# Optimization experiments

Measured on AMD Instinct MI355X. Metric: run time of the kernel, lower is better.

Reference implementation:

```python
import jax, jax.numpy as jnp
import numpy as np

N = 50000      # nodes
E = 800000     # edges (avg degree 16)
F_IN = 128
HID = 128
C = 40
EPS = 1e-5     # BatchNorm1d eps


def setup_inputs() -> dict:
    key = jax.random.key(0)
    ks = jax.random.split(key, 8)

    def glorot(k, shape):
        lim = np.sqrt(6.0 / (shape[0] + shape[1])).astype(np.float32)
        return jax.random.uniform(k, shape, jnp.float32, -lim, lim)

    inp = {
        "features": jax.random.normal(ks[0], (N, F_IN), jnp.float32),
        "edge_index": jax.random.randint(ks[1], (2, E), 0, N, jnp.int32),
        "W1": glorot(ks[2], (F_IN, HID)), "b1": jnp.zeros((HID,), jnp.float32),
        "gamma1": jnp.ones((HID,), jnp.float32), "beta1": jnp.zeros((HID,), jnp.float32),
        "W2": glorot(ks[3], (HID, HID)), "b2": jnp.zeros((HID,), jnp.float32),
        "gamma2": jnp.ones((HID,), jnp.float32), "beta2": jnp.zeros((HID,), jnp.float32),
        "W3": glorot(ks[4], (HID, C)), "b3": jnp.zeros((C,), jnp.float32),
    }
    return inp


def _gcn_norm(edge_index):
    # Add self-loops and compute symmetric normalization D^-1/2 (A+I) D^-1/2
    loops = jnp.arange(N, dtype=edge_index.dtype)
    src = jnp.concatenate([edge_index[0], loops])
    dst = jnp.concatenate([edge_index[1], loops])
    deg = jax.ops.segment_sum(jnp.ones((E + N,), jnp.float32), dst, num_segments=N)
    dinv = jax.lax.rsqrt(jnp.maximum(deg, 1.0))
    return src, dst, dinv[src] * dinv[dst]  # per-edge norm coefficient


def _gcn_conv(x, W, b, src, dst, norm):
    h = x @ W                                   # [N, out]
    msg = h[src] * norm[:, None]                # gather + scale, [E+N, out]
    return jax.ops.segment_sum(msg, dst, num_segments=N) + b


def _bn(x, gamma, beta):
    # training-mode BatchNorm1d over the node axis (biased variance)
    mu = jnp.mean(x, axis=0)
    var = jnp.mean(jnp.square(x - mu), axis=0)
    return (x - mu) * jax.lax.rsqrt(var + EPS) * gamma + beta


def reference(features, edge_index, W1, b1, gamma1, beta1, W2, b2, gamma2, beta2, W3, b3):
    src, dst, norm = _gcn_norm(edge_index)
    h = jax.nn.relu(_bn(_gcn_conv(features, W1, b1, src, dst, norm), gamma1, beta1))
    h = jax.nn.relu(_bn(_gcn_conv(h, W2, b2, src, dst, norm), gamma2, beta2))
    h = _gcn_conv(h, W3, b3, src, dst, norm)
    return jax.nn.log_softmax(h, axis=-1)
```

## Files before the change

### kernel.cpp

```cpp
#include <hip/hip_runtime.h>
#include <math.h>

#define FEAT 128
#define NCLS 40
#define BN_EPS 1e-5f
#define CAP 64

typedef unsigned short u16;
typedef unsigned int u32;
typedef __attribute__((ext_vector_type(8))) short bf16x8;
typedef __attribute__((ext_vector_type(4))) float f32x4;

__device__ inline u32 f2b2(float a, float b) {
    u32 ua = __float_as_uint(a), ub = __float_as_uint(b);
    ua = (ua + 0x7fffu + ((ua >> 16) & 1u)) >> 16;
    ub = (ub + 0x7fffu + ((ub >> 16) & 1u)) >> 16;
    return ua | (ub << 16);
}
__device__ inline u16 f2b1(float a) {
    u32 ua = __float_as_uint(a);
    return (u16)((ua + 0x7fffu + ((ua >> 16) & 1u)) >> 16);
}
__device__ inline float b2f(u16 u) { return __uint_as_float((u32)u << 16); }
__device__ inline float4 b4fv(ushort4 u) {
    return make_float4(b2f(u.x), b2f(u.y), b2f(u.z), b2f(u.w));
}
__device__ inline float blo(u32 u) { return __uint_as_float(u << 16); }
__device__ inline float bhi(u32 u) { return __uint_as_float(u & 0xffff0000u); }

__device__ inline void b8acc(uint4 u, float w, float* a) {
    a[0] = fmaf(w, blo(u.x), a[0]); a[1] = fmaf(w, bhi(u.x), a[1]);
    a[2] = fmaf(w, blo(u.y), a[2]); a[3] = fmaf(w, bhi(u.y), a[3]);
    a[4] = fmaf(w, blo(u.z), a[4]); a[5] = fmaf(w, bhi(u.z), a[5]);
    a[6] = fmaf(w, blo(u.w), a[6]); a[7] = fmaf(w, bhi(u.w), a[7]);
}

#define WT_PITCH 136


__device__ inline void stage_wt(const float* __restrict__ W, u16* Wt) {
    const float4* W4 = (const float4*)W;
#pragma unroll
    for (int i = 0; i < 16; ++i) {
        int li = threadIdx.x + i * 256;
        int k = li >> 5;
        int n0 = (li & 31) * 4;
        float4 w = W4[li];
        Wt[(n0 + 0) * WT_PITCH + ((k + ((n0 + 0 & 3) << 5)) & 127)] = f2b1(w.x);
        Wt[(n0 + 1) * WT_PITCH + ((k + ((n0 + 1 & 3) << 5)) & 127)] = f2b1(w.y);
        Wt[(n0 + 2) * WT_PITCH + ((k + ((n0 + 2 & 3) << 5)) & 127)] = f2b1(w.z);
        Wt[(n0 + 3) * WT_PITCH + ((k + ((n0 + 3 & 3) << 5)) & 127)] = f2b1(w.w);
    }
}

__device__ inline void mfma_core(const u16* Wt, const bf16x8* bfrag,
                                 u16* __restrict__ Y, int node, int M, int nl, int quad) {
    f32x4 acc[8];
#pragma unroll
    for (int nt = 0; nt < 8; ++nt) acc[nt] = (f32x4){0.f, 0.f, 0.f, 0.f};
#pragma unroll
    for (int s = 0; s < 4; ++s) {
#pragma unroll
        for (int nt = 0; nt < 8; ++nt) {
            int nrow = nt * 16 + nl;
            int kk = ((s * 32 + quad * 8) + ((nl & 3) << 5)) & 127;
            uint4 aw = *(const uint4*)&Wt[nrow * WT_PITCH + kk];
            bf16x8 af = *(bf16x8*)&aw;
            acc[nt] = __builtin_amdgcn_mfma_f32_16x16x32_bf16(af, bfrag[s], acc[nt], 0, 0, 0);
        }
    }
    if (node < M) {
#pragma unroll
        for (int nt = 0; nt < 8; ++nt) {
            uint2 o;
            o.x = f2b2(acc[nt][0], acc[nt][1]);
            o.y = f2b2(acc[nt][2], acc[nt][3]);
            *(uint2*)&Y[(size_t)node * 128 + nt * 16 + quad * 4] = o;
        }
    }
}


__global__ __launch_bounds__(256) void k_l1_fill(
    const float* __restrict__ X, const float* __restrict__ W, u16* __restrict__ Y, int M,
    const int* __restrict__ src, const int* __restrict__ dst,
    int* __restrict__ cnt, int* __restrict__ col, int E,
    int gemmBlocks, int nchunks)
{
    __shared__ __align__(16) u16 Wt[128 * WT_PITCH];

    if ((int)blockIdx.x < gemmBlocks) {
        stage_wt(W, Wt);
        __syncthreads();

        int wv = threadIdx.x >> 6;
        int lane = threadIdx.x & 63;
        int nl = lane & 15, quad = lane >> 4;
        int node = blockIdx.x * 64 + wv * 16 + nl;

        bf16x8 bfrag[4];
        if (node < M) {
            const float4* xr = (const float4*)(X + (size_t)node * 128);
#pragma unroll
            for (int s = 0; s < 4; ++s) {
                float4 xa = xr[s * 8 + quad * 2];
                float4 xb = xr[s * 8 + quad * 2 + 1];
                uint4 bu;
                bu.x = f2b2(xa.x, xa.y); bu.y = f2b2(xa.z, xa.w);
                bu.z = f2b2(xb.x, xb.y); bu.w = f2b2(xb.z, xb.w);
                bfrag[s] = *(bf16x8*)&bu;
            }
        } else {
            uint4 z = make_uint4(0, 0, 0, 0);
#pragma unroll
            for (int s = 0; s < 4; ++s) bfrag[s] = *(bf16x8*)&z;
        }
        mfma_core(Wt, bfrag, Y, node, M, nl, quad);
    } else {
        int fb = blockIdx.x - gemmBlocks;
        int part = fb & 7;
        int chunk = fb >> 3;
        int lo = (int)(((long long)M * part) >> 3);
        int hi = (int)(((long long)M * (part + 1)) >> 3);
        int per = ((E + nchunks - 1) / nchunks + 3) & ~3;
        int e0 = chunk * per;
        int e1 = e0 + per; if (e1 > E) e1 = E;

        for (int eb = e0 + (int)threadIdx.x * 4; eb < e1; eb += 1024) {
            if (eb + 4 <= e1) {
                int4 d4 = *(const int4*)(dst + eb);
                int dd[4] = {d4.x, d4.y, d4.z, d4.w};
#pragma unroll
                for (int k = 0; k < 4; ++k) {
                    int d = dd[k];
                    if (d >= lo && d < hi) {
                        int c = atomicAdd(&cnt[d], 1);
                        if (c < CAP) col[(size_t)d * CAP + c] = src[eb + k];
                    }
                }
            } else {
                for (int e = eb; e < e1; ++e) {
                    int d = dst[e];
                    if (d >= lo && d < hi) {
                        int c = atomicAdd(&cnt[d], 1);
                        if (c < CAP) col[(size_t)d * CAP + c] = src[e];
                    }
                }
            }
        }
    }
}


__global__ __launch_bounds__(256) void k_prep(
    const int* __restrict__ cnt, const int* __restrict__ col,
    float* __restrict__ wsrc, int n)
{
    int s = blockIdx.x * 256 + threadIdx.x;
    int node = s >> 6;
    if (node >= n) return;
    int j = s & (CAP - 1);
    int c = cnt[node];
    int deg = c < CAP ? c : CAP;
    if (j < deg) {
        int sc = col[(size_t)node * CAP + j];
        wsrc[(size_t)node * CAP + j] = rsqrtf((float)(cnt[sc] + 1));
    }
}


__global__ __launch_bounds__(256) void k_mfma_l2(
    const u16* __restrict__ X, const float* __restrict__ W,
    const float* __restrict__ sums, const float* __restrict__ gamma,
    const float* __restrict__ beta, u16* __restrict__ Y, int M)
{
    __shared__ __align__(16) u16 Wt[128 * WT_PITCH];
    __shared__ __align__(16) float scs[128], shs[128];

    if (threadIdx.x < 128) {
        int f = threadIdx.x;
        float inv_n = 1.f / (float)M;
        float mu = sums[f] * inv_n;
        float var = sums[128 + f] * inv_n - mu * mu;
        float rs = rsqrtf(var + BN_EPS);
        float sc = gamma[f] * rs;
        scs[f] = sc;
        shs[f] = beta[f] - mu * sc;
    }
    stage_wt(W, Wt);
    __syncthreads();

    int wv = threadIdx.x >> 6;
    int lane = threadIdx.x & 63;
    int nl = lane & 15, quad = lane >> 4;
    int node = blockIdx.x * 64 + wv * 16 + nl;

    bf16x8 bfrag[4];
    if (node < M) {
        const uint4* xr = (const uint4*)(X + (size_t)node * 128);
#pragma unroll
        for (int s = 0; s < 4; ++s) {
            int k0 = s * 32 + quad * 8;
            uint4 xu = xr[s * 4 + quad];
            float4 sc0 = *(const float4*)&scs[k0];
            float4 sc1 = *(const float4*)&scs[k0 + 4];
            float4 sh0 = *(const float4*)&shs[k0];
            float4 sh1 = *(const float4*)&shs[k0 + 4];
            float v0 = fmaxf(fmaf(blo(xu.x), sc0.x, sh0.x), 0.f);
            float v1 = fmaxf(fmaf(bhi(xu.x), sc0.y, sh0.y), 0.f);
            float v2 = fmaxf(fmaf(blo(xu.y), sc0.z, sh0.z), 0.f);
            float v3 = fmaxf(fmaf(bhi(xu.y), sc0.w, sh0.w), 0.f);
            float v4 = fmaxf(fmaf(blo(xu.z), sc1.x, sh1.x), 0.f);
            float v5 = fmaxf(fmaf(bhi(xu.z), sc1.y, sh1.y), 0.f);
            float v6 = fmaxf(fmaf(blo(xu.w), sc1.z, sh1.z), 0.f);
            float v7 = fmaxf(fmaf(bhi(xu.w), sc1.w, sh1.w), 0.f);
            uint4 bu;
            bu.x = f2b2(v0, v1); bu.y = f2b2(v2, v3);
            bu.z = f2b2(v4, v5); bu.w = f2b2(v6, v7);
            bfrag[s] = *(bf16x8*)&bu;
        }
    } else {
        uint4 z = make_uint4(0, 0, 0, 0);
#pragma unroll
        for (int s = 0; s < 4; ++s) bfrag[s] = *(bf16x8*)&z;
    }
    mfma_core(Wt, bfrag, Y, node, M, nl, quad);
}


__global__ __launch_bounds__(256) void k_gemm40(
    const u16* __restrict__ X, const float* __restrict__ W,
    const float* __restrict__ sums, const float* __restrict__ gamma,
    const float* __restrict__ beta, u16* __restrict__ Y, int M)
{
    __shared__ float Ws[128 * 40];
    __shared__ __align__(16) float scs[128], shs[128];
    __shared__ float Xs[32 * 260];

    int t = threadIdx.x;
    int row0 = blockIdx.x * 256;
    int tx = t & 3, ty = t >> 2;

    if (t < 128) {
        float inv_n = 1.f / (float)M;
        float mu = sums[t] * inv_n;
        float var = sums[128 + t] * inv_n - mu * mu;
        float rs = rsqrtf(var + BN_EPS);
        float sc = gamma[t] * rs;
        scs[t] = sc;
        shs[t] = beta[t] - mu * sc;
    }
    {
        const float4* W4 = (const float4*)W;
        float4* Ws4 = (float4*)Ws;
#pragma unroll
        for (int i = 0; i < 5; ++i) Ws4[t + i * 256] = W4[t + i * 256];
    }

    float acc[4][10];
#pragma unroll
    for (int r = 0; r < 4; ++r)
#pragma unroll
        for (int c = 0; c < 10; ++c) acc[r][c] = 0.f;

    for (int k0 = 0; k0 < 128; k0 += 32) {
        __syncthreads();
        {
            int rr = t >> 3;
            int kc = (t & 7) * 4;
            float4 sc = *(const float4*)&scs[k0 + kc];
            float4 sh = *(const float4*)&shs[k0 + kc];
#pragma unroll
            for (int p = 0; p < 8; ++p) {
                int r = rr + p * 32;
                int grow = row0 + r;
                float4 v = make_float4(0.f, 0.f, 0.f, 0.f);
                if (grow < M) v = b4fv(*(const ushort4*)(X + (size_t)grow * 128 + k0 + kc));
                v.x = fmaxf(fmaf(v.x, sc.x, sh.x), 0.f);
                v.y = fmaxf(fmaf(v.y, sc.y, sh.y), 0.f);
                v.z = fmaxf(fmaf(v.z, sc.z, sh.z), 0.f);
                v.w = fmaxf(fmaf(v.w, sc.w, sh.w), 0.f);
                Xs[(kc + 0) * 260 + r] = v.x;
                Xs[(kc + 1) * 260 + r] = v.y;
                Xs[(kc + 2) * 260 + r] = v.z;
                Xs[(kc + 3) * 260 + r] = v.w;
            }
        }
        __syncthreads();
#pragma unroll 8
        for (int kk = 0; kk < 32; ++kk) {
            const float4 xv = *(const float4*)&Xs[kk * 260 + ty * 4];
            const float xr[4] = {xv.x, xv.y, xv.z, xv.w};
            float wc[10];
#pragma unroll
            for (int c = 0; c < 5; ++c) {
                float2 w2 = *(const float2*)&Ws[(k0 + kk) * 40 + tx * 10 + c * 2];
                wc[c * 2] = w2.x; wc[c * 2 + 1] = w2.y;
            }
#pragma unroll
            for (int r = 0; r < 4; ++r)
#pragma unroll
                for (int c = 0; c < 10; ++c)
                    acc[r][c] = fmaf(xr[r], wc[c], acc[r][c]);
        }
    }

#pragma unroll
    for (int r = 0; r < 4; ++r) {
        int grow = row0 + ty * 4 + r;
        if (grow < M) {
            u32* yp = (u32*)(Y + (size_t)grow * 40 + tx * 10);
#pragma unroll
            for (int c = 0; c < 5; ++c)
                yp[c] = f2b2(acc[r][c * 2], acc[r][c * 2 + 1]);
        }
    }
}


__global__ __launch_bounds__(256) void k_agg128(
    const u16* __restrict__ t, const int* __restrict__ cnt,
    const int* __restrict__ col, const float* __restrict__ wsrc,
    const float* __restrict__ bias, u16* __restrict__ out, int n)
{
    int wid = threadIdx.x >> 4;
    int lane = threadIdx.x & 15;
    int i = blockIdx.x * 16 + wid;
    if (i >= n) return;
    int c = cnt[i];
    int deg = c < CAP ? c : CAP;
    int beg = i * CAP, end = beg + deg;
    float di = rsqrtf((float)(c + 1));

    float a[8];
    {
        uint4 su = ((const uint4*)(t + (size_t)i * 128))[lane];
        a[0] = di * blo(su.x); a[1] = di * bhi(su.x);
        a[2] = di * blo(su.y); a[3] = di * bhi(su.y);
        a[4] = di * blo(su.z); a[5] = di * bhi(su.z);
        a[6] = di * blo(su.w); a[7] = di * bhi(su.w);
    }

    int j = beg;
    for (; j + 7 < end; j += 8) {
        int s[8]; float w[8]; uint4 v[8];
#pragma unroll
        for (int k = 0; k < 8; ++k) { s[k] = col[j + k]; w[k] = wsrc[j + k]; }
#pragma unroll
        for (int k = 0; k < 8; ++k) v[k] = ((const uint4*)(t + (size_t)s[k] * 128))[lane];
#pragma unroll
        for (int k = 0; k < 8; ++k) b8acc(v[k], w[k], a);
    }
    for (; j < end; ++j) {
        float w0 = wsrc[j];
        uint4 v = ((const uint4*)(t + (size_t)col[j] * 128))[lane];
        b8acc(v, w0, a);
    }

    float4 bA = ((const float4*)bias)[lane * 2];
    float4 bB = ((const float4*)bias)[lane * 2 + 1];
    uint4 o;
    o.x = f2b2(fmaf(di, a[0], bA.x), fmaf(di, a[1], bA.y));
    o.y = f2b2(fmaf(di, a[2], bA.z), fmaf(di, a[3], bA.w));
    o.z = f2b2(fmaf(di, a[4], bB.x), fmaf(di, a[5], bB.y));
    o.w = f2b2(fmaf(di, a[6], bB.z), fmaf(di, a[7], bB.w));
    ((uint4*)(out + (size_t)i * 128))[lane] = o;
}


__global__ __launch_bounds__(256) void k_bnstats(const u16* __restrict__ a,
                                                 float* __restrict__ sums, int n) {
    int lane = threadIdx.x & 15;
    int rt = threadIdx.x >> 4;
    float s[8], q[8];
#pragma unroll
    for (int k = 0; k < 8; ++k) { s[k] = 0.f; q[k] = 0.f; }

    for (int i = blockIdx.x * 16 + rt; i < n; i += gridDim.x * 16) {
        uint4 u = ((const uint4*)(a + (size_t)i * 128))[lane];
        float v[8] = {blo(u.x), bhi(u.x), blo(u.y), bhi(u.y),
                      blo(u.z), bhi(u.z), blo(u.w), bhi(u.w)};
#pragma unroll
        for (int k = 0; k < 8; ++k) { s[k] += v[k]; q[k] = fmaf(v[k], v[k], q[k]); }
    }

    __shared__ float red[16][128];
#pragma unroll
    for (int k = 0; k < 8; ++k) red[rt][lane * 8 + k] = s[k];
    __syncthreads();
    if (threadIdx.x < 128) {
        float v = 0.f;
#pragma unroll
        for (int w = 0; w < 16; ++w) v += red[w][threadIdx.x];
        atomicAdd(&sums[threadIdx.x], v);
    }
    __syncthreads();
#pragma unroll
    for (int k = 0; k < 8; ++k) red[rt][lane * 8 + k] = q[k];
    __syncthreads();
    if (threadIdx.x < 128) {
        float v = 0.f;
#pragma unroll
        for (int w = 0; w < 16; ++w) v += red[w][threadIdx.x];
        atomicAdd(&sums[128 + threadIdx.x], v);
    }
}


__global__ __launch_bounds__(256) void k_agg40(
    const u16* __restrict__ t, const int* __restrict__ cnt,
    const int* __restrict__ col, const float* __restrict__ wsrc,
    const float* __restrict__ bias, float* __restrict__ out, int n)
{
    int i = blockIdx.x * 32 + (threadIdx.x >> 3);
    if (i >= n) return;
    int l = threadIdx.x & 7;
    bool act = l < 5;
    int c = cnt[i];
    int deg = c < CAP ? c : CAP;
    int beg = i * CAP, end = beg + deg;
    float di = rsqrtf((float)(c + 1));

    float a[8] = {0.f, 0.f, 0.f, 0.f, 0.f, 0.f, 0.f, 0.f};
    if (act) {
        uint4 su = ((const uint4*)(t + (size_t)i * NCLS))[l];
        a[0] = di * blo(su.x); a[1] = di * bhi(su.x);
        a[2] = di * blo(su.y); a[3] = di * bhi(su.y);
        a[4] = di * blo(su.z); a[5] = di * bhi(su.z);
        a[6] = di * blo(su.w); a[7] = di * bhi(su.w);
    }
    int j = beg;
    for (; j + 7 < end; j += 8) {
        int s[8]; float w[8]; uint4 v[8];
#pragma unroll
        for (int k = 0; k < 8; ++k) { s[k] = col[j + k]; w[k] = wsrc[j + k]; }
#pragma unroll
        for (int k = 0; k < 8; ++k)
            v[k] = act ? ((const uint4*)(t + (size_t)s[k] * NCLS))[l]
                       : make_uint4(0, 0, 0, 0);
#pragma unroll
        for (int k = 0; k < 8; ++k) b8acc(v[k], w[k], a);
    }
    for (; j < end; ++j) {
        float w0 = wsrc[j];
        uint4 v = act ? ((const uint4*)(t + (size_t)col[j] * NCLS))[l]
                      : make_uint4(0, 0, 0, 0);
        b8acc(v, w0, a);
    }

    float v[8];
    float m = -INFINITY;
    if (act) {
        float4 b0 = *(const float4*)(bias + l * 8);
        float4 b1 = *(const float4*)(bias + l * 8 + 4);
        v[0] = fmaf(di, a[0], b0.x); v[1] = fmaf(di, a[1], b0.y);
        v[2] = fmaf(di, a[2], b0.z); v[3] = fmaf(di, a[3], b0.w);
        v[4] = fmaf(di, a[4], b1.x); v[5] = fmaf(di, a[5], b1.y);
        v[6] = fmaf(di, a[6], b1.z); v[7] = fmaf(di, a[7], b1.w);
#pragma unroll
        for (int k = 0; k < 8; ++k) m = fmaxf(m, v[k]);
    }
#pragma unroll
    for (int d = 1; d < 8; d <<= 1) m = fmaxf(m, __shfl_xor(m, d, 8));
    float es = 0.f;
    if (act) {
#pragma unroll
        for (int k = 0; k < 8; ++k) es += expf(v[k] - m);
    }
#pragma unroll
    for (int d = 1; d < 8; d <<= 1) es += __shfl_xor(es, d, 8);
    float ls = logf(es);
    if (act) {
        float4 o0, o1;
        o0.x = v[0] - m - ls; o0.y = v[1] - m - ls;
        o0.z = v[2] - m - ls; o0.w = v[3] - m - ls;
        o1.x = v[4] - m - ls; o1.y = v[5] - m - ls;
        o1.z = v[6] - m - ls; o1.w = v[7] - m - ls;
        *(float4*)(out + (size_t)i * NCLS + l * 8) = o0;
        *(float4*)(out + (size_t)i * NCLS + l * 8 + 4) = o1;
    }
}


extern "C" void kernel_launch(void* const* d_in, const int* in_sizes, int n_in,
                              void* d_out, int out_size, void* d_ws, size_t ws_size,
                              hipStream_t stream) {
    const float* features = (const float*)d_in[0];
    const int* edge_index = (const int*)d_in[1];
    const float* W1 = (const float*)d_in[2];
    const float* b1 = (const float*)d_in[3];
    const float* gamma1 = (const float*)d_in[4];
    const float* beta1 = (const float*)d_in[5];
    const float* W2 = (const float*)d_in[6];
    const float* b2 = (const float*)d_in[7];
    const float* gamma2 = (const float*)d_in[8];
    const float* beta2 = (const float*)d_in[9];
    const float* W3 = (const float*)d_in[10];
    const float* b3 = (const float*)d_in[11];
    float* out = (float*)d_out;

    int n = in_sizes[0] / FEAT;
    int E = in_sizes[1] / 2;

    char* p = (char*)d_ws;
    auto alloc = [&](size_t bytes) -> void* {
        void* r = (void*)p;
        p += (bytes + 255) & ~(size_t)255;
        return r;
    };
    int* cnt     = (int*)alloc((size_t)n * 4);
    float* sums  = (float*)alloc(512 * 4);
    size_t zspan = (size_t)((char*)(sums + 512) - (char*)cnt);
    int* colb    = (int*)alloc((size_t)n * CAP * 4);
    float* wsrc  = (float*)alloc((size_t)n * CAP * 4);
    u16* hb      = (u16*)alloc((size_t)n * 128 * 2);
    u16* ab      = (u16*)alloc((size_t)n * 128 * 2);

    float* sums1 = sums;
    float* sums2 = sums + 256;

    const int* e_src = edge_index;
    const int* e_dst = edge_index + E;

    int gb64 = (n + 63) / 64;
    int gb16 = (n + 15) / 16;
    int gb32 = (n + 31) / 32;

    hipMemsetAsync(cnt, 0, zspan, stream);
    int nchunks = 160;
    k_l1_fill<<<gb64 + nchunks * 8, 256, 0, stream>>>(features, W1, hb, n,
                                                      e_src, e_dst, cnt, colb, E,
                                                      gb64, nchunks);
    k_prep<<<(n * CAP + 255) / 256, 256, 0, stream>>>(cnt, colb, wsrc, n);

    k_agg128<<<gb16, 256, 0, stream>>>(hb, cnt, colb, wsrc, b1, ab, n);
    k_bnstats<<<512, 256, 0, stream>>>(ab, sums1, n);

    k_mfma_l2<<<gb64, 256, 0, stream>>>(ab, W2, sums1, gamma1, beta1, hb, n);
    k_agg128<<<gb16, 256, 0, stream>>>(hb, cnt, colb, wsrc, b2, ab, n);
    k_bnstats<<<512, 256, 0, stream>>>(ab, sums2, n);

    k_gemm40<<<(n + 255) / 256, 256, 0, stream>>>(ab, W3, sums2, gamma2, beta2, hb, n);
    k_agg40<<<gb32, 256, 0, stream>>>(hb, cnt, colb, wsrc, b3, out, n);
}
```

Measured before the change: 334.3 us.

## Drop per-edge weight precompute and store W in MFMA fragment order

Removes the k_prep kernel and the n*64 float wsrc buffer. The aggregation kernels now compute each source node's normalization on the fly from cnt, gathering cnt[src] alongside the feature row. This trades a kernel launch and the wsrc write/read traffic for extra scattered 4-byte loads and rsqrt calls inside the aggregation loops. Separately, the weight tile in LDS is laid out in MFMA fragment order, so each lane does one contiguous 16-byte read per fragment instead of using the padded, swizzled pitch.

```diff
diff --git a/kernel.cpp b/kernel.cpp
--- a/kernel.cpp
+++ b/kernel.cpp
@@ -35,8 +35,6 @@
     a[6] = fmaf(w, blo(u.w), a[6]); a[7] = fmaf(w, bhi(u.w), a[7]);
 }
 
-#define WT_PITCH 136
-
 
 __device__ inline void stage_wt(const float* __restrict__ W, u16* Wt) {
     const float4* W4 = (const float4*)W;
@@ -45,16 +43,20 @@
         int li = threadIdx.x + i * 256;
         int k = li >> 5;
         int n0 = (li & 31) * 4;
+        int s = k >> 5, quad = (k >> 3) & 3, koff = k & 7;
+        int nt = n0 >> 4, nl0 = n0 & 15;
+        int base = ((s * 8 + nt) * 64 + quad * 16) * 8 + koff;
         float4 w = W4[li];
-        Wt[(n0 + 0) * WT_PITCH + ((k + ((n0 + 0 & 3) << 5)) & 127)] = f2b1(w.x);
-        Wt[(n0 + 1) * WT_PITCH + ((k + ((n0 + 1 & 3) << 5)) & 127)] = f2b1(w.y);
-        Wt[(n0 + 2) * WT_PITCH + ((k + ((n0 + 2 & 3) << 5)) & 127)] = f2b1(w.z);
-        Wt[(n0 + 3) * WT_PITCH + ((k + ((n0 + 3 & 3) << 5)) & 127)] = f2b1(w.w);
+        Wt[base + (nl0 + 0) * 8] = f2b1(w.x);
+        Wt[base + (nl0 + 1) * 8] = f2b1(w.y);
+        Wt[base + (nl0 + 2) * 8] = f2b1(w.z);
+        Wt[base + (nl0 + 3) * 8] = f2b1(w.w);
     }
 }
 
 __device__ inline void mfma_core(const u16* Wt, const bf16x8* bfrag,
                                  u16* __restrict__ Y, int node, int M, int nl, int quad) {
+    int lane = quad * 16 + nl;
     f32x4 acc[8];
 #pragma unroll
     for (int nt = 0; nt < 8; ++nt) acc[nt] = (f32x4){0.f, 0.f, 0.f, 0.f};
@@ -62,9 +64,7 @@
     for (int s = 0; s < 4; ++s) {
 #pragma unroll
         for (int nt = 0; nt < 8; ++nt) {
-            int nrow = nt * 16 + nl;
-            int kk = ((s * 32 + quad * 8) + ((nl & 3) << 5)) & 127;
-            uint4 aw = *(const uint4*)&Wt[nrow * WT_PITCH + kk];
+            uint4 aw = ((const uint4*)Wt)[(s * 8 + nt) * 64 + lane];
             bf16x8 af = *(bf16x8*)&aw;
             acc[nt] = __builtin_amdgcn_mfma_f32_16x16x32_bf16(af, bfrag[s], acc[nt], 0, 0, 0);
         }
@@ -87,7 +87,7 @@
     int* __restrict__ cnt, int* __restrict__ col, int E,
     int gemmBlocks, int nchunks)
 {
-    __shared__ __align__(16) u16 Wt[128 * WT_PITCH];
+    __shared__ __align__(16) u16 Wt[128 * 128];
 
     if ((int)blockIdx.x < gemmBlocks) {
         stage_wt(W, Wt);
@@ -152,29 +152,12 @@
 }
 
 
-__global__ __launch_bounds__(256) void k_prep(
-    const int* __restrict__ cnt, const int* __restrict__ col,
-    float* __restrict__ wsrc, int n)
-{
-    int s = blockIdx.x * 256 + threadIdx.x;
-    int node = s >> 6;
-    if (node >= n) return;
-    int j = s & (CAP - 1);
-    int c = cnt[node];
-    int deg = c < CAP ? c : CAP;
-    if (j < deg) {
-        int sc = col[(size_t)node * CAP + j];
-        wsrc[(size_t)node * CAP + j] = rsqrtf((float)(cnt[sc] + 1));
-    }
-}
-
-
 __global__ __launch_bounds__(256) void k_mfma_l2(
     const u16* __restrict__ X, const float* __restrict__ W,
     const float* __restrict__ sums, const float* __restrict__ gamma,
     const float* __restrict__ beta, u16* __restrict__ Y, int M)
 {
-    __shared__ __align__(16) u16 Wt[128 * WT_PITCH];
+    __shared__ __align__(16) u16 Wt[128 * 128];
     __shared__ __align__(16) float scs[128], shs[128];
 
     if (threadIdx.x < 128) {
@@ -320,8 +303,8 @@
 
 __global__ __launch_bounds__(256) void k_agg128(
     const u16* __restrict__ t, const int* __restrict__ cnt,
-    const int* __restrict__ col, const float* __restrict__ wsrc,
-    const float* __restrict__ bias, u16* __restrict__ out, int n)
+    const int* __restrict__ col, const float* __restrict__ bias,
+    u16* __restrict__ out, int n)
 {
     int wid = threadIdx.x >> 4;
     int lane = threadIdx.x & 15;
@@ -343,17 +326,21 @@
 
     int j = beg;
     for (; j + 7 < end; j += 8) {
-        int s[8]; float w[8]; uint4 v[8];
-#pragma unroll
-        for (int k = 0; k < 8; ++k) { s[k] = col[j + k]; w[k] = wsrc[j + k]; }
-#pragma unroll
-        for (int k = 0; k < 8; ++k) v[k] = ((const uint4*)(t + (size_t)s[k] * 128))[lane];
-#pragma unroll
-        for (int k = 0; k < 8; ++k) b8acc(v[k], w[k], a);
+        int s[8]; int sc[8]; uint4 v[8];
+#pragma unroll
+        for (int k = 0; k < 8; ++k) s[k] = col[j + k];
+#pragma unroll
+        for (int k = 0; k < 8; ++k) {
+            sc[k] = cnt[s[k]];
+            v[k] = ((const uint4*)(t + (size_t)s[k] * 128))[lane];
+        }
+#pragma unroll
+        for (int k = 0; k < 8; ++k) b8acc(v[k], rsqrtf((float)(sc[k] + 1)), a);
     }
     for (; j < end; ++j) {
-        float w0 = wsrc[j];
-        uint4 v = ((const uint4*)(t + (size_t)col[j] * 128))[lane];
+        int s0 = col[j];
+        float w0 = rsqrtf((float)(cnt[s0] + 1));
+        uint4 v = ((const uint4*)(t + (size_t)s0 * 128))[lane];
         b8acc(v, w0, a);
     }
 
@@ -409,8 +396,8 @@
 
 __global__ __launch_bounds__(256) void k_agg40(
     const u16* __restrict__ t, const int* __restrict__ cnt,
-    const int* __restrict__ col, const float* __restrict__ wsrc,
-    const float* __restrict__ bias, float* __restrict__ out, int n)
+    const int* __restrict__ col, const float* __restrict__ bias,
+    float* __restrict__ out, int n)
 {
     int i = blockIdx.x * 32 + (threadIdx.x >> 3);
     if (i >= n) return;
@@ -431,19 +418,22 @@
     }
     int j = beg;
     for (; j + 7 < end; j += 8) {
-        int s[8]; float w[8]; uint4 v[8];
-#pragma unroll
-        for (int k = 0; k < 8; ++k) { s[k] = col[j + k]; w[k] = wsrc[j + k]; }
-#pragma unroll
-        for (int k = 0; k < 8; ++k)
+        int s[8]; int sc[8]; uint4 v[8];
+#pragma unroll
+        for (int k = 0; k < 8; ++k) s[k] = col[j + k];
+#pragma unroll
+        for (int k = 0; k < 8; ++k) {
+            sc[k] = cnt[s[k]];
             v[k] = act ? ((const uint4*)(t + (size_t)s[k] * NCLS))[l]
                        : make_uint4(0, 0, 0, 0);
-#pragma unroll
-        for (int k = 0; k < 8; ++k) b8acc(v[k], w[k], a);
+        }
+#pragma unroll
+        for (int k = 0; k < 8; ++k) b8acc(v[k], rsqrtf((float)(sc[k] + 1)), a);
     }
     for (; j < end; ++j) {
-        float w0 = wsrc[j];
-        uint4 v = act ? ((const uint4*)(t + (size_t)col[j] * NCLS))[l]
+        int s0 = col[j];
+        float w0 = rsqrtf((float)(cnt[s0] + 1));
+        uint4 v = act ? ((const uint4*)(t + (size_t)s0 * NCLS))[l]
                       : make_uint4(0, 0, 0, 0);
         b8acc(v, w0, a);
     }
@@ -512,7 +502,6 @@
     float* sums  = (float*)alloc(512 * 4);
     size_t zspan = (size_t)((char*)(sums + 512) - (char*)cnt);
     int* colb    = (int*)alloc((size_t)n * CAP * 4);
-    float* wsrc  = (float*)alloc((size_t)n * CAP * 4);
     u16* hb      = (u16*)alloc((size_t)n * 128 * 2);
     u16* ab      = (u16*)alloc((size_t)n * 128 * 2);
 
@@ -531,15 +520,14 @@
     k_l1_fill<<<gb64 + nchunks * 8, 256, 0, stream>>>(features, W1, hb, n,
                                                       e_src, e_dst, cnt, colb, E,
                                                       gb64, nchunks);
-    k_prep<<<(n * CAP + 255) / 256, 256, 0, stream>>>(cnt, colb, wsrc, n);
-
-    k_agg128<<<gb16, 256, 0, stream>>>(hb, cnt, colb, wsrc, b1, ab, n);
+
+    k_agg128<<<gb16, 256, 0, stream>>>(hb, cnt, colb, b1, ab, n);
     k_bnstats<<<512, 256, 0, stream>>>(ab, sums1, n);
 
     k_mfma_l2<<<gb64, 256, 0, stream>>>(ab, W2, sums1, gamma1, beta1, hb, n);
-    k_agg128<<<gb16, 256, 0, stream>>>(hb, cnt, colb, wsrc, b2, ab, n);
+    k_agg128<<<gb16, 256, 0, stream>>>(hb, cnt, colb, b2, ab, n);
     k_bnstats<<<512, 256, 0, stream>>>(ab, sums2, n);
 
     k_gemm40<<<(n + 255) / 256, 256, 0, stream>>>(ab, W3, sums2, gamma2, beta2, hb, n);
-    k_agg40<<<gb32, 256, 0, stream>>>(hb, cnt, colb, wsrc, b3, out, n);
-}
+    k_agg40<<<gb32, 256, 0, stream>>>(hb, cnt, colb, b3, out, n);
+}
```

Result: faster. 320.0 us (-4.3%).
